# Performance work log

Hardware: AMD Instinct MI355X
Metric: run time of the kernel (lower is better)

Reference implementation:

```python
import jax, jax.numpy as jnp
import numpy as np

D = 1024
H = 16
HD = D // H
T = 2048
B = 2
HID = 4 * D
EPS = 1e-5


def setup_inputs() -> dict:
    key = jax.random.key(0)
    ks = jax.random.split(key, 8)
    s = lambda fan_in: 1.0 / np.sqrt(fan_in)
    return {
        "x": jax.random.normal(ks[0], (B, T, D), dtype=jnp.float32),
        "ln1_g": jnp.ones((D,), jnp.float32),
        "ln1_b": jnp.zeros((D,), jnp.float32),
        "Wqkv": jax.random.uniform(ks[1], (D, 3 * D), jnp.float32, -s(D), s(D)),
        "bqkv": jnp.zeros((3 * D,), jnp.float32),
        "Wout": jax.random.uniform(ks[2], (D, D), jnp.float32, -s(D), s(D)),
        "bout": jnp.zeros((D,), jnp.float32),
        "ln2_g": jnp.ones((D,), jnp.float32),
        "ln2_b": jnp.zeros((D,), jnp.float32),
        "W1": jax.random.uniform(ks[3], (D, HID), jnp.float32, -s(D), s(D)),
        "b1": jnp.zeros((HID,), jnp.float32),
        "W2": jax.random.uniform(ks[4], (HID, D), jnp.float32, -s(HID), s(HID)),
        "b2": jnp.zeros((D,), jnp.float32),
    }


def _layernorm(h, g, b):
    mu = jnp.mean(h, axis=-1, keepdims=True)
    var = jnp.mean(jnp.square(h - mu), axis=-1, keepdims=True)
    return (h - mu) * jax.lax.rsqrt(var + EPS) * g + b


def reference(x, ln1_g, ln1_b, Wqkv, bqkv, Wout, bout, ln2_g, ln2_b, W1, b1, W2, b2):
    b, t, d = x.shape
    scale = 1.0 / np.sqrt(HD)

    # --- attention (pre-LN) ---
    h = _layernorm(x, ln1_g, ln1_b)
    qkv = h @ Wqkv + bqkv                      # [b, t, 3d]
    q, k, v = jnp.split(qkv, 3, axis=-1)
    q = q.reshape(b, t, H, HD)
    k = k.reshape(b, t, H, HD)
    v = v.reshape(b, t, H, HD)
    scores = jnp.einsum("bqhd,bkhd->bhqk", q, k) * scale  # [b, h, t, t]
    causal = jnp.tril(jnp.ones((t, t), dtype=bool))
    scores = jnp.where(causal, scores, -jnp.inf)
    attn = jax.nn.softmax(scores, axis=-1)
    out = jnp.einsum("bhqk,bkhd->bqhd", attn, v).reshape(b, t, d)
    x = x + (out @ Wout + bout)

    # --- MLP (pre-LN) ---
    h = _layernorm(x, ln2_g, ln2_b)
    h = jax.nn.gelu(h @ W1 + b1, approximate=False)
    x = x + (h @ W2 + b2)
    return x
```

## Files before the change

kernel.cpp:

```cpp
#include <hip/hip_runtime.h>
#include <hip/hip_bf16.h>
#include <math.h>

#define DD 1024
#define TT 2048
#define BB 2
#define HH 16
#define HDIM 64
#define HIDD 4096

typedef __attribute__((ext_vector_type(4))) float f32x4;
typedef __attribute__((ext_vector_type(8))) __bf16 bf16x8;
typedef __attribute__((ext_vector_type(4))) __bf16 bf16x4;

#define MF16 __builtin_amdgcn_mfma_f32_16x16x32_bf16

__device__ __forceinline__ void gload_lds16(const void* g, void* l) {
  __builtin_amdgcn_global_load_lds(
      (const __attribute__((address_space(1))) void*)g,
      (__attribute__((address_space(3))) void*)l, 16, 0, 0);
}

__global__ __launch_bounds__(256) void castAll(const float* __restrict__ Wqkv,
                                               const float* __restrict__ Wout,
                                               const float* __restrict__ W1,
                                               const float* __restrict__ W2,
                                               __bf16* __restrict__ WqkvT,
                                               __bf16* __restrict__ WoutT,
                                               __bf16* __restrict__ W1T,
                                               __bf16* __restrict__ W2T) {
  const int id = blockIdx.x;
  const float* W;
  __bf16* Wt;
  int K, N, gx, local;
  if (id < 768)        { W = Wqkv; Wt = WqkvT; K = 1024; N = 3072; gx = 48; local = id; }
  else if (id < 1024)  { W = Wout; Wt = WoutT; K = 1024; N = 1024; gx = 16; local = id - 768; }
  else if (id < 2048)  { W = W1;   Wt = W1T;   K = 1024; N = 4096; gx = 64; local = id - 1024; }
  else                 { W = W2;   Wt = W2T;   K = 4096; N = 1024; gx = 16; local = id - 2048; }
  const int n0 = (local % gx) * 64, k0 = (local / gx) * 64;
  __shared__ float t[64][65];
#pragma unroll
  for (int e = 0; e < 16; ++e) {
    int idx = e * 256 + threadIdx.x;
    int rr = idx >> 6, cc = idx & 63;
    t[rr][cc] = W[(size_t)(k0 + rr) * N + n0 + cc];
  }
  __syncthreads();
#pragma unroll
  for (int e = 0; e < 16; ++e) {
    int idx = e * 256 + threadIdx.x;
    int rr = idx >> 6, cc = idx & 63;
    Wt[(size_t)(n0 + rr) * K + k0 + cc] = (__bf16)t[cc][rr];
  }
}

__global__ __launch_bounds__(256) void ln_fwd(const float* __restrict__ x,
                                              const float* __restrict__ gamma,
                                              const float* __restrict__ beta,
                                              __bf16* __restrict__ out) {
  const int wave = threadIdx.x >> 6, lane = threadIdx.x & 63;
  const int row = blockIdx.x * 4 + wave;
  const float* xr = x + (size_t)row * DD;
  float4 v[4];
  float s = 0.0f, ss = 0.0f;
#pragma unroll
  for (int c = 0; c < 4; ++c) {
    v[c] = reinterpret_cast<const float4*>(xr)[c * 64 + lane];
    s += v[c].x + v[c].y + v[c].z + v[c].w;
    ss += v[c].x * v[c].x + v[c].y * v[c].y + v[c].z * v[c].z + v[c].w * v[c].w;
  }
#pragma unroll
  for (int m = 1; m <= 32; m <<= 1) { s += __shfl_xor(s, m); ss += __shfl_xor(ss, m); }
  const float mu = s * (1.0f / DD);
  const float rs = rsqrtf(ss * (1.0f / DD) - mu * mu + 1e-5f);
#pragma unroll
  for (int c = 0; c < 4; ++c) {
    const float4 gm = reinterpret_cast<const float4*>(gamma)[c * 64 + lane];
    const float4 bt = reinterpret_cast<const float4*>(beta)[c * 64 + lane];
    bf16x4 o;
    o[0] = (__bf16)((v[c].x - mu) * rs * gm.x + bt.x);
    o[1] = (__bf16)((v[c].y - mu) * rs * gm.y + bt.y);
    o[2] = (__bf16)((v[c].z - mu) * rs * gm.z + bt.z);
    o[3] = (__bf16)((v[c].w - mu) * rs * gm.w + bt.w);
    *reinterpret_cast<bf16x4*>(out + (size_t)row * DD + (c * 64 + lane) * 4) = o;
  }
}

template <int MODE, int MAP = 0>
__global__ __launch_bounds__(512, 1) void gemm8(const __bf16* __restrict__ A,
                                                const __bf16* __restrict__ Bt,
                                                const float* __restrict__ bias,
                                                void* __restrict__ out0,
                                                __bf16* __restrict__ q1,
                                                __bf16* __restrict__ q2,
                                                __bf16* __restrict__ q3,
                                                int N, int K, int kchunk) {
  const int tid = threadIdx.x;
  const int wid = tid >> 6, lane = tid & 63;
  const int g = lane >> 4, r = lane & 15;
  const int wrh = wid >> 2;
  const int wc = (wid & 3) * 64;

  int bm, bn, kbase, zz;
  if constexpr (MODE == 3) {
    const int L = blockIdx.x;
    const int xcd = L & 7, idx = L >> 3;
    zz = xcd >> 1;
    bm = (((xcd & 1) << 3) + (idx >> 2)) * 256;
    bn = (idx & 3) * 256;
    kbase = zz * kchunk;
  } else if constexpr (MAP == 1) {
    const int L = blockIdx.x;
    const int xcd = L & 7, idx = L >> 3;
    bm = (((xcd & 1) << 3) + (idx >> 2)) * 256;
    bn = (((xcd >> 1) << 2) + (idx & 3)) * 256;
    kbase = 0;
    zz = 0;
  } else {
    const int gx = gridDim.x;
    const int nwg = gx * gridDim.y;
    const int orig = blockIdx.y * gx + blockIdx.x;
    const int swz = (orig & 7) * (nwg >> 3) + (orig >> 3);
    const int bn4 = swz & 3;
    const int bmt = (swz >> 2) % gx;
    const int bng = (swz >> 2) / gx;
    bm = bmt * 256;
    bn = (bng * 4 + bn4) * 256;
    kbase = 0;
    zz = 0;
  }

  const int NT = kchunk >> 6;
  const __bf16* Asrc = A + (size_t)bm * K + kbase;
  const __bf16* Bsrc = Bt + (size_t)bn * K + kbase;

  __shared__ __bf16 lds[2][4][8192];

  f32x4 acc[8][4] = {};
  bf16x8 bfr[4][2];

  auto STG = [&](int ab, int h, int kt) {
    const __bf16* src = (ab ? Bsrc : Asrc) + (size_t)h * 128 * K;
    char* dst = (char*)&lds[kt & 1][ab * 2 + h][0];
#pragma unroll
    for (int gl = 0; gl < 2; ++gl) {
      const int o = gl * 8192 + wid * 1024 + lane * 16;
      const int row = o >> 7;
      const int cbs = (o & 127) ^ (((row >> 2) & 1) << 5);
      gload_lds16((const char*)src + (size_t)row * (K * 2) + kt * 128 + cbs,
                  dst + gl * 8192 + wid * 1024);
    }
  };
  auto DSA = [&](int s, int mi, int kk) -> bf16x8 {
    return *(const bf16x8*)((const char*)&lds[s][wrh][0] + (mi * 16 + r) * 128 +
                            ((kk * 64 + g * 16) ^ ((r & 4) << 3)));
  };
  auto DSB = [&](int s, int nj, int kk) -> bf16x8 {
    const int rt = wc + nj * 16 + r;
    return *(const bf16x8*)((const char*)&lds[s][2 + (rt >> 7)][0] + (rt & 127) * 128 +
                            ((kk * 64 + g * 16) ^ ((r & 4) << 3)));
  };

#define PH(S, Q, STAGE_STMT, WAIT_STMT)                                        \
  {                                                                            \
    if (Q == 0) {                                                              \
      _Pragma("unroll") for (int nj = 0; nj < 4; ++nj) {                       \
        bfr[nj][0] = DSB(S, nj, 0);                                            \
        bfr[nj][1] = DSB(S, nj, 1);                                            \
      }                                                                        \
    }                                                                          \
    bf16x8 a00 = DSA(S, 2 * Q, 0), a01 = DSA(S, 2 * Q, 1);                     \
    bf16x8 a10 = DSA(S, 2 * Q + 1, 0), a11 = DSA(S, 2 * Q + 1, 1);             \
    STAGE_STMT;                                                                \
    WAIT_STMT;                                                                 \
    __builtin_amdgcn_s_barrier();                                              \
    asm volatile("s_waitcnt lgkmcnt(0)" ::: "memory");                         \
    __builtin_amdgcn_s_setprio(1);                                             \
    _Pragma("unroll") for (int nj = 0; nj < 4; ++nj) {                         \
      acc[2 * Q][nj] = MF16(a00, bfr[nj][0], acc[2 * Q][nj], 0, 0, 0);         \
      acc[2 * Q][nj] = MF16(a01, bfr[nj][1], acc[2 * Q][nj], 0, 0, 0);         \
      acc[2 * Q + 1][nj] = MF16(a10, bfr[nj][0], acc[2 * Q + 1][nj], 0, 0, 0); \
      acc[2 * Q + 1][nj] = MF16(a11, bfr[nj][1], acc[2 * Q + 1][nj], 0, 0, 0); \
    }                                                                          \
    __builtin_amdgcn_s_setprio(0);                                             \
    __builtin_amdgcn_s_barrier();                                              \
  }

  STG(1, 0, 0); STG(1, 1, 0); STG(0, 0, 0); STG(0, 1, 0);
  STG(1, 0, 1); STG(1, 1, 1); STG(0, 0, 1);
  asm volatile("s_waitcnt vmcnt(6)" ::: "memory");
  __builtin_amdgcn_s_barrier();

  const int NI = NT >> 1;
  for (int i = 0; i < NI; ++i) {
    const int k2 = 2 * i + 2, k3 = 2 * i + 3;
    const bool nl = (i + 1 < NI);
    PH(0, 0, { STG(0, 1, 2 * i + 1); }, {});
    PH(0, 1, { if (nl) STG(1, 0, k2); }, {});
    PH(0, 2, { if (nl) STG(1, 1, k2); }, {});
    PH(0, 3, { if (nl) STG(0, 0, k2); },
       { if (nl) asm volatile("s_waitcnt vmcnt(6)" ::: "memory");
         else    asm volatile("s_waitcnt vmcnt(0)" ::: "memory"); });
    PH(1, 0, { if (nl) STG(0, 1, k2); }, {});
    PH(1, 1, { if (nl) STG(1, 0, k3); }, {});
    PH(1, 2, { if (nl) STG(1, 1, k3); }, {});
    PH(1, 3, { if (nl) STG(0, 0, k3); },
       { if (nl) asm volatile("s_waitcnt vmcnt(6)" ::: "memory"); });
  }
#undef PH

  const int row0 = bm + wrh * 128 + g * 4;
  const int col0 = bn + wc + r;
#pragma unroll
  for (int mi = 0; mi < 8; ++mi) {
#pragma unroll
    for (int nj = 0; nj < 4; ++nj) {
      const int col = col0 + nj * 16;
      float bv = 0.0f;
      if constexpr (MODE != 3) bv = bias[col];
#pragma unroll
      for (int i4 = 0; i4 < 4; ++i4) {
        const int rowg = row0 + mi * 16 + i4;
        const size_t idx = (size_t)rowg * N + col;
        const float v = acc[mi][nj][i4];
        if constexpr (MODE == 0) {
          ((__bf16*)out0)[idx] = (__bf16)(v + bv);
        } else if constexpr (MODE == 2) {
          const float t = v + bv;
          const float u2 = t * (1.5957691216f + t * t * 0.0713548163f);
          ((__bf16*)out0)[idx] = (__bf16)(t * __builtin_amdgcn_rcpf(1.0f + __expf(-u2)));
        } else {
          if (zz == 0) {
            ((float*)out0)[idx] = v;
          } else {
            __bf16* p = (zz == 1 ? q1 : (zz == 2 ? q2 : q3));
            p[idx] = (__bf16)v;
          }
        }
      }
    }
  }
}

__global__ __launch_bounds__(256) void reduceW2(const __bf16* __restrict__ p1,
                                                const __bf16* __restrict__ p2,
                                                const __bf16* __restrict__ p3,
                                                const float* __restrict__ x1,
                                                const float* __restrict__ b2,
                                                float* __restrict__ out) {
  const size_t i8 = ((size_t)blockIdx.x * 256 + threadIdx.x) * 8;
  const int col0 = (int)(i8 & 1023);
  bf16x8 a = *(const bf16x8*)(p1 + i8);
  bf16x8 b = *(const bf16x8*)(p2 + i8);
  bf16x8 c = *(const bf16x8*)(p3 + i8);
  float4 o0 = *(const float4*)(out + i8);
  float4 o1 = *(const float4*)(out + i8 + 4);
  const float4 xv0 = *(const float4*)(x1 + i8);
  const float4 xv1 = *(const float4*)(x1 + i8 + 4);
  const float4 bb0 = *(const float4*)(b2 + col0);
  const float4 bb1 = *(const float4*)(b2 + col0 + 4);
  float* op0 = (float*)&o0;
  float* op1 = (float*)&o1;
  const float* xp0 = (const float*)&xv0;
  const float* xp1 = (const float*)&xv1;
  const float* bp0 = (const float*)&bb0;
  const float* bp1 = (const float*)&bb1;
#pragma unroll
  for (int j = 0; j < 4; ++j)
    op0[j] += xp0[j] + bp0[j] + (float)a[j] + (float)b[j] + (float)c[j];
#pragma unroll
  for (int j = 0; j < 4; ++j)
    op1[j] += xp1[j] + bp1[j] + (float)a[4 + j] + (float)b[4 + j] + (float)c[4 + j];
  *(float4*)(out + i8) = o0;
  *(float4*)(out + i8 + 4) = o1;
}

template <int MODE>
__global__ __launch_bounds__(256) void gemm_bt(const __bf16* __restrict__ A,
                                               const __bf16* __restrict__ Bt,
                                               const float* __restrict__ bias,
                                               const float* __restrict__ resid,
                                               void* __restrict__ Cout,
                                               int M, int N, int K) {
  __shared__ __bf16 As[128 * 32];
  __shared__ __bf16 Bs[128 * 32];
  const int tid = threadIdx.x;
  const int wave = tid >> 6, lane = tid & 63;
  const int g = lane >> 4, r = lane & 15;
  const int gx = gridDim.x;
  const int nwg = gx * gridDim.y;
  const int orig = blockIdx.y * gx + blockIdx.x;
  const int swz = (orig & 7) * (nwg >> 3) + (orig >> 3);
  const int bn4 = swz & 3;
  const int bmt = (swz >> 2) % gx;
  const int bng = (swz >> 2) / gx;
  const int bm = bmt * 128;
  const int bn = (bng * 4 + bn4) * 128;
  const int wr = (wave >> 1) * 64, wc = (wave & 1) * 64;
  f32x4 acc[4][4] = {};

  const int off0 = wave * 2048 + lane * 16;
  const int off1 = off0 + 1024;
  const int sr0 = off0 >> 6, sk0 = (off0 & 63) >> 1;
  const int sr1 = off1 >> 6, sk1 = (off1 & 63) >> 1;
  const __bf16* gA0 = A + (size_t)(bm + sr0) * K + sk0;
  const __bf16* gA1 = A + (size_t)(bm + sr1) * K + sk1;
  const __bf16* gB0 = Bt + (size_t)(bn + sr0) * K + sk0;
  const __bf16* gB1 = Bt + (size_t)(bn + sr1) * K + sk1;
  char* lA0 = (char*)As + wave * 2048;
  char* lA1 = lA0 + 1024;
  char* lB0 = (char*)Bs + wave * 2048;
  char* lB1 = lB0 + 1024;

  for (int k0 = 0; k0 < K; k0 += 32) {
    gload_lds16(gA0 + k0, lA0);
    gload_lds16(gA1 + k0, lA1);
    gload_lds16(gB0 + k0, lB0);
    gload_lds16(gB1 + k0, lB1);
    __syncthreads();
    bf16x8 af[4], bf[4];
#pragma unroll
    for (int mi = 0; mi < 4; ++mi)
      af[mi] = *reinterpret_cast<const bf16x8*>(&As[(wr + mi * 16 + r) * 32 + g * 8]);
#pragma unroll
    for (int ni = 0; ni < 4; ++ni)
      bf[ni] = *reinterpret_cast<const bf16x8*>(&Bs[(wc + ni * 16 + r) * 32 + g * 8]);
    __builtin_amdgcn_s_setprio(1);
#pragma unroll
    for (int mi = 0; mi < 4; ++mi)
#pragma unroll
      for (int ni = 0; ni < 4; ++ni)
        acc[mi][ni] = MF16(af[mi], bf[ni], acc[mi][ni], 0, 0, 0);
    __builtin_amdgcn_s_setprio(0);
    __syncthreads();
  }

  const int row0 = bm + wr + 4 * g;
  const int col0 = bn + wc + r;
#pragma unroll
  for (int mi = 0; mi < 4; ++mi) {
#pragma unroll
    for (int ni = 0; ni < 4; ++ni) {
      const int col = col0 + ni * 16;
      const float bv = bias[col];
#pragma unroll
      for (int i = 0; i < 4; ++i) {
        const int row = row0 + mi * 16 + i;
        const size_t idx = (size_t)row * N + col;
        float v = acc[mi][ni][i] + bv;
        if (MODE == 0) {
          ((__bf16*)Cout)[idx] = (__bf16)v;
        } else if (MODE == 1) {
          ((float*)Cout)[idx] = v + resid[idx];
        } else {
          const float u2 = v * (1.5957691216f + v * v * 0.0713548163f);
          const float gl = v * __builtin_amdgcn_rcpf(1.0f + __expf(-u2));
          ((__bf16*)Cout)[idx] = (__bf16)gl;
        }
      }
    }
  }
}

__global__ __launch_bounds__(256) void vtrans(const __bf16* __restrict__ qkv,
                                              __bf16* __restrict__ vtg) {
  const int bh = blockIdx.y, b = bh >> 4, h = bh & 15;
  const int t0 = blockIdx.x * 64;
  const int tid = threadIdx.x, wave = tid >> 6, lane = tid & 63;
  __shared__ __bf16 tile[64 * 64];
#pragma unroll
  for (int e = 0; e < 2; ++e) {
    const int gid = e * 256 + tid;
    const int row = gid >> 3, d0 = (gid & 7) * 8;
    bf16x8 v = *reinterpret_cast<const bf16x8*>(
        qkv + (size_t)(b * TT + t0 + row) * 3072 + 2048 + h * 64 + d0);
    const int slot = (d0 >> 3) ^ (row & 7);
    *reinterpret_cast<bf16x8*>((char*)tile + row * 128 + slot * 16) = v;
  }
  __syncthreads();
  const int d = lane;
#pragma unroll
  for (int e = 0; e < 2; ++e) {
    const int k0 = (wave * 2 + e) * 8;
    bf16x8 o;
#pragma unroll
    for (int j = 0; j < 8; ++j) {
      const int row = k0 + j;
      o[j] = *(const __bf16*)((const char*)tile + row * 128 +
                              (((d >> 3) ^ (row & 7)) << 4) + (d & 7) * 2);
    }
    *reinterpret_cast<bf16x8*>(&vtg[((size_t)bh * 64 + d) * 2048 + t0 + k0]) = o;
  }
}

__device__ __forceinline__ void stage_kv(const __bf16* __restrict__ src_row0, int rstride,
                                         int wave, int lane, char* tile) {
#pragma unroll
  for (int qq = 0; qq < 2; ++qq) {
    const int o = wave * 2048 + qq * 1024 + lane * 16;
    const int p = o >> 12, row = (o >> 6) & 63, cb = (o >> 4) & 3;
    gload_lds16(src_row0 + (size_t)row * rstride + p * 32 + cb * 8,
                tile + wave * 2048 + qq * 1024);
  }
}

__global__ __launch_bounds__(256) void attn_fwd(const __bf16* __restrict__ qkv,
                                                const __bf16* __restrict__ vtg,
                                                __bf16* __restrict__ atto) {
  const int orig = blockIdx.y * gridDim.x + blockIdx.x;
  const int swz = (orig & 7) * 64 + (orig >> 3);
  const int bh = swz >> 4;
  const int j = swz & 15;
  const int b = bh >> 4, h = bh & 15;
  const int tid = threadIdx.x;
  const int wave = tid >> 6, lane = tid & 63;
  const int g = lane >> 4, r = lane & 15;

  __shared__ __bf16 Qs[2 * 64 * 32];
  __shared__ __bf16 Ks[2][2 * 64 * 32];
  __shared__ __bf16 Vs[2][2 * 64 * 32];
  __shared__ __bf16 Pl[4][2 * 16 * 32];

  const __bf16* ksrc = qkv + (size_t)(b * TT) * 3072 + 1024 + h * 64;
  const __bf16* vsrc = vtg + (size_t)bh * 64 * 2048;
  const float C2 = 0.18033688011112042f;

  for (int ph = 0; ph < 2; ++ph) {
    const int qt = ph ? (31 - j) : j;
    const int q0 = qt * 64;
    stage_kv(qkv + (size_t)(b * TT + q0) * 3072 + h * 64, 3072, wave, lane, (char*)Qs);
    stage_kv(ksrc, 3072, wave, lane, (char*)Ks[0]);
    stage_kv(vsrc, 2048, wave, lane, (char*)Vs[0]);

    f32x4 oacc[4] = {};
    float m_s[4], l_s[4];
#pragma unroll
    for (int i = 0; i < 4; ++i) { m_s[i] = -1e30f; l_s[i] = 0.0f; }

    const int nt = qt + 1;
    int cur = 0;
    for (int t = 0; t < nt; ++t) {
      const int kv0 = t * 64;
      __syncthreads();
      if (t + 1 < nt) {
        stage_kv(ksrc + (size_t)(kv0 + 64) * 3072, 3072, wave, lane, (char*)Ks[cur ^ 1]);
        stage_kv(vsrc + kv0 + 64, 2048, wave, lane, (char*)Vs[cur ^ 1]);
      }
      bf16x8 qf[2];
#pragma unroll
      for (int kp = 0; kp < 2; ++kp)
        qf[kp] = *reinterpret_cast<const bf16x8*>(&Qs[kp * 2048 + (wave * 16 + r) * 32 + g * 8]);
      f32x4 s[4];
#pragma unroll
      for (int cn = 0; cn < 4; ++cn) s[cn] = f32x4{0.f, 0.f, 0.f, 0.f};
      __builtin_amdgcn_s_setprio(1);
#pragma unroll
      for (int cn = 0; cn < 4; ++cn)
#pragma unroll
        for (int kp = 0; kp < 2; ++kp) {
          bf16x8 bk = *reinterpret_cast<const bf16x8*>(
              &Ks[cur][kp * 2048 + (cn * 16 + r) * 32 + g * 8]);
          s[cn] = MF16(qf[kp], bk, s[cn], 0, 0, 0);
        }
      __builtin_amdgcn_s_setprio(0);
      const int rowg = q0 + wave * 16 + 4 * g;
      float pm[4];
#pragma unroll
      for (int i = 0; i < 4; ++i) pm[i] = -1e30f;
      if (kv0 + 63 > q0 + wave * 16) {
#pragma unroll
        for (int cn = 0; cn < 4; ++cn) {
          const int colg = kv0 + cn * 16 + r;
#pragma unroll
          for (int i = 0; i < 4; ++i) {
            float v = s[cn][i] * C2;
            v = (colg > rowg + i) ? -1e30f : v;
            s[cn][i] = v;
            pm[i] = fmaxf(pm[i], v);
          }
        }
      } else {
#pragma unroll
        for (int cn = 0; cn < 4; ++cn)
#pragma unroll
          for (int i = 0; i < 4; ++i) {
            const float v = s[cn][i] * C2;
            s[cn][i] = v;
            pm[i] = fmaxf(pm[i], v);
          }
      }
      const int upd = __any((pm[0] > m_s[0] + 8.0f) || (pm[1] > m_s[1] + 8.0f) ||
                            (pm[2] > m_s[2] + 8.0f) || (pm[3] > m_s[3] + 8.0f));
      if (upd) {
#pragma unroll
        for (int i = 0; i < 4; ++i) {
          pm[i] = fmaxf(pm[i], __shfl_xor(pm[i], 1));
          pm[i] = fmaxf(pm[i], __shfl_xor(pm[i], 2));
          pm[i] = fmaxf(pm[i], __shfl_xor(pm[i], 4));
          pm[i] = fmaxf(pm[i], __shfl_xor(pm[i], 8));
          const float mn = fmaxf(m_s[i], pm[i]);
          const float sf = __builtin_amdgcn_exp2f(m_s[i] - mn);
          m_s[i] = mn;
          l_s[i] *= sf;
#pragma unroll
          for (int ni = 0; ni < 4; ++ni) oacc[ni][i] *= sf;
        }
      }
#pragma unroll
      for (int cn = 0; cn < 4; ++cn)
#pragma unroll
        for (int i = 0; i < 4; ++i) {
          const float p = __builtin_amdgcn_exp2f(s[cn][i] - m_s[i]);
          s[cn][i] = p;
          l_s[i] += p;
        }
#pragma unroll
      for (int cn = 0; cn < 4; ++cn)
#pragma unroll
        for (int i = 0; i < 4; ++i) {
          const int row = 4 * g + i;
          const int byteoff = (cn >> 1) * 1024 +
              ((row * 64 + (cn & 1) * 32 + r * 2) ^ ((row & 7) << 4));
          *(__bf16*)((char*)&Pl[wave][0] + byteoff) = (__bf16)s[cn][i];
        }
      bf16x8 pa[2];
#pragma unroll
      for (int kp = 0; kp < 2; ++kp) {
        const int byteoff = kp * 1024 + ((r * 64 + g * 16) ^ ((r & 7) << 4));
        pa[kp] = *reinterpret_cast<const bf16x8*>((const char*)&Pl[wave][0] + byteoff);
      }
      __builtin_amdgcn_s_setprio(1);
#pragma unroll
      for (int ni = 0; ni < 4; ++ni)
#pragma unroll
        for (int kp = 0; kp < 2; ++kp) {
          bf16x8 bv = *reinterpret_cast<const bf16x8*>(
              &Vs[cur][kp * 2048 + (ni * 16 + r) * 32 + g * 8]);
          oacc[ni] = MF16(pa[kp], bv, oacc[ni], 0, 0, 0);
        }
      __builtin_amdgcn_s_setprio(0);
      cur ^= 1;
    }

#pragma unroll
    for (int i = 0; i < 4; ++i) {
      float l = l_s[i];
      l += __shfl_xor(l, 1);
      l += __shfl_xor(l, 2);
      l += __shfl_xor(l, 4);
      l += __shfl_xor(l, 8);
      const float inv = 1.0f / l;
      const size_t rowo = (size_t)(b * TT + q0 + wave * 16 + 4 * g + i) * DD + h * 64;
#pragma unroll
      for (int ni = 0; ni < 4; ++ni)
        atto[rowo + ni * 16 + r] = (__bf16)(oacc[ni][i] * inv);
    }
    __syncthreads();
  }
}

extern "C" void kernel_launch(void* const* d_in, const int* in_sizes, int n_in,
                              void* d_out, int out_size, void* d_ws, size_t ws_size,
                              hipStream_t stream) {
  const float* x     = (const float*)d_in[0];
  const float* ln1_g = (const float*)d_in[1];
  const float* ln1_b = (const float*)d_in[2];
  const float* Wqkv  = (const float*)d_in[3];
  const float* bqkv  = (const float*)d_in[4];
  const float* Wout  = (const float*)d_in[5];
  const float* bout  = (const float*)d_in[6];
  const float* ln2_g = (const float*)d_in[7];
  const float* ln2_b = (const float*)d_in[8];
  const float* W1    = (const float*)d_in[9];
  const float* b1    = (const float*)d_in[10];
  const float* W2    = (const float*)d_in[11];
  const float* b2    = (const float*)d_in[12];
  float* out = (float*)d_out;

  char* ws = (char*)d_ws;
  const size_t MB = 1024 * 1024;
  __bf16* WqkvT = (__bf16*)(ws);
  __bf16* WoutT = (__bf16*)(ws + 6 * MB);
  __bf16* W1T   = (__bf16*)(ws + 8 * MB);
  __bf16* W2T   = (__bf16*)(ws + 16 * MB);
  float*  x1    = (float*)(ws + 24 * MB);
  __bf16* vtg   = (__bf16*)(ws + 24 * MB);
  __bf16* hbuf  = (__bf16*)(ws + 40 * MB);
  __bf16* qkvb  = (__bf16*)(ws + 48 * MB);
  __bf16* atto  = (__bf16*)(ws + 72 * MB);
  __bf16* mlp1  = (__bf16*)(ws + 48 * MB);
  __bf16* p1b   = (__bf16*)(ws);
  __bf16* p2b   = (__bf16*)(ws + 8 * MB);
  __bf16* p3b   = (__bf16*)(ws + 40 * MB);

  castAll<<<3072, 256, 0, stream>>>(Wqkv, Wout, W1, W2, WqkvT, WoutT, W1T, W2T);

  ln_fwd<<<1024, 256, 0, stream>>>(x, ln1_g, ln1_b, hbuf);
  gemm8<0><<<dim3(16, 12), 512, 0, stream>>>(hbuf, WqkvT, bqkv, qkvb,
                                             nullptr, nullptr, nullptr, 3072, 1024, 1024);
  vtrans<<<dim3(32, 32), 256, 0, stream>>>(qkvb, vtg);
  attn_fwd<<<dim3(16, 32), 256, 0, stream>>>(qkvb, vtg, atto);
  gemm_bt<1><<<dim3(32, 8), 256, 0, stream>>>(atto, WoutT, bout, x, x1, 4096, 1024, 1024);

  ln_fwd<<<1024, 256, 0, stream>>>(x1, ln2_g, ln2_b, hbuf);
  gemm8<2, 1><<<256, 512, 0, stream>>>(hbuf, W1T, b1, mlp1,
                                       nullptr, nullptr, nullptr, 4096, 1024, 1024);
  gemm8<3><<<dim3(256, 1), 512, 0, stream>>>(mlp1, W2T, nullptr, out,
                                             p1b, p2b, p3b, 1024, 4096, 1024);
  reduceW2<<<2048, 256, 0, stream>>>(p1b, p2b, p3b, x1, b2, out);
}
```

Before: 232.8 us.

## Replace split-K W2 GEMM with dedicated single-buffered 128x256 tile kernel

Moves the split-K down-projection GEMM off the heavily pipelined 256x256 gemm8 path and into a new gemm_w2 kernel. The new kernel uses 256-thread blocks with 128x256 tiles and a K-step of 32, and launches 512 blocks instead of 256 to get more blocks per CU and better occupancy. It loses the double-buffered LDS pipeline and the swizzled layout, synchronises twice per K step, and its unswizzled LDS reads may cause bank conflicts. gemm8 is simplified by dropping the split-K mode.

Result: slower. 280.3 us (+20.4%).

```diff
diff --git a/kernel.cpp b/kernel.cpp
--- a/kernel.cpp
+++ b/kernel.cpp
@@ -91,9 +91,6 @@
                                                 const __bf16* __restrict__ Bt,
                                                 const float* __restrict__ bias,
                                                 void* __restrict__ out0,
-                                                __bf16* __restrict__ q1,
-                                                __bf16* __restrict__ q2,
-                                                __bf16* __restrict__ q3,
                                                 int N, int K, int kchunk) {
   const int tid = threadIdx.x;
   const int wid = tid >> 6, lane = tid & 63;
@@ -101,21 +98,12 @@
   const int wrh = wid >> 2;
   const int wc = (wid & 3) * 64;
 
-  int bm, bn, kbase, zz;
-  if constexpr (MODE == 3) {
-    const int L = blockIdx.x;
-    const int xcd = L & 7, idx = L >> 3;
-    zz = xcd >> 1;
-    bm = (((xcd & 1) << 3) + (idx >> 2)) * 256;
-    bn = (idx & 3) * 256;
-    kbase = zz * kchunk;
-  } else if constexpr (MAP == 1) {
+  int bm, bn;
+  if constexpr (MAP == 1) {
     const int L = blockIdx.x;
     const int xcd = L & 7, idx = L >> 3;
     bm = (((xcd & 1) << 3) + (idx >> 2)) * 256;
     bn = (((xcd >> 1) << 2) + (idx & 3)) * 256;
-    kbase = 0;
-    zz = 0;
   } else {
     const int gx = gridDim.x;
     const int nwg = gx * gridDim.y;
@@ -126,13 +114,11 @@
     const int bng = (swz >> 2) / gx;
     bm = bmt * 256;
     bn = (bng * 4 + bn4) * 256;
-    kbase = 0;
-    zz = 0;
   }
 
   const int NT = kchunk >> 6;
-  const __bf16* Asrc = A + (size_t)bm * K + kbase;
-  const __bf16* Bsrc = Bt + (size_t)bn * K + kbase;
+  const __bf16* Asrc = A + (size_t)bm * K;
+  const __bf16* Bsrc = Bt + (size_t)bn * K;
 
   __shared__ __bf16 lds[2][4][8192];
 
@@ -216,8 +202,7 @@
 #pragma unroll
     for (int nj = 0; nj < 4; ++nj) {
       const int col = col0 + nj * 16;
-      float bv = 0.0f;
-      if constexpr (MODE != 3) bv = bias[col];
+      const float bv = bias[col];
 #pragma unroll
       for (int i4 = 0; i4 < 4; ++i4) {
         const int rowg = row0 + mi * 16 + i4;
@@ -225,17 +210,99 @@
         const float v = acc[mi][nj][i4];
         if constexpr (MODE == 0) {
           ((__bf16*)out0)[idx] = (__bf16)(v + bv);
-        } else if constexpr (MODE == 2) {
+        } else {
           const float t = v + bv;
           const float u2 = t * (1.5957691216f + t * t * 0.0713548163f);
           ((__bf16*)out0)[idx] = (__bf16)(t * __builtin_amdgcn_rcpf(1.0f + __expf(-u2)));
+        }
+      }
+    }
+  }
+}
+
+__global__ __launch_bounds__(256) void gemm_w2(const __bf16* __restrict__ A,
+                                               const __bf16* __restrict__ Bt,
+                                               void* __restrict__ out0,
+                                               __bf16* __restrict__ q1,
+                                               __bf16* __restrict__ q2,
+                                               __bf16* __restrict__ q3) {
+  const int K = 4096, N = 1024;
+  __shared__ __bf16 As[128 * 32];
+  __shared__ __bf16 Bs[256 * 32];
+  const int tid = threadIdx.x;
+  const int wave = tid >> 6, lane = tid & 63;
+  const int g = lane >> 4, r = lane & 15;
+
+  const int L = blockIdx.x;
+  const int xcd = L & 7, idx = L >> 3;
+  const int zz = xcd >> 1;
+  const int bm = (((xcd & 1) << 4) + (idx >> 2)) * 128;
+  const int bn = (idx & 3) * 256;
+  const int kbase = zz * 1024;
+
+  f32x4 acc[4][8] = {};
+
+  const int off0 = wave * 2048 + lane * 16;
+  const int off1 = off0 + 1024;
+  const int sr0 = off0 >> 6, sk0 = (off0 & 63) >> 1;
+  const int sr1 = off1 >> 6, sk1 = (off1 & 63) >> 1;
+  const __bf16* gA0 = A + (size_t)(bm + sr0) * K + kbase + sk0;
+  const __bf16* gA1 = A + (size_t)(bm + sr1) * K + kbase + sk1;
+  char* lA0 = (char*)As + wave * 2048;
+  char* lA1 = lA0 + 1024;
+  const __bf16* gB[4];
+  char* lB[4];
+#pragma unroll
+  for (int q = 0; q < 4; ++q) {
+    const int ob = wave * 4096 + q * 1024 + lane * 16;
+    const int rb = ob >> 6, kb = (ob & 63) >> 1;
+    gB[q] = Bt + (size_t)(bn + rb) * K + kbase + kb;
+    lB[q] = (char*)Bs + wave * 4096 + q * 1024;
+  }
+
+  const int mh = wave >> 1;
+  const int nh = wave & 1;
+
+  for (int k0 = 0; k0 < 1024; k0 += 32) {
+    gload_lds16(gA0 + k0, lA0);
+    gload_lds16(gA1 + k0, lA1);
+#pragma unroll
+    for (int q = 0; q < 4; ++q) gload_lds16(gB[q] + k0, lB[q]);
+    __syncthreads();
+    bf16x8 af[4], bf[8];
+#pragma unroll
+    for (int mi = 0; mi < 4; ++mi)
+      af[mi] = *reinterpret_cast<const bf16x8*>(&As[(mh * 64 + mi * 16 + r) * 32 + g * 8]);
+#pragma unroll
+    for (int ni = 0; ni < 8; ++ni)
+      bf[ni] = *reinterpret_cast<const bf16x8*>(&Bs[(nh * 128 + ni * 16 + r) * 32 + g * 8]);
+    __builtin_amdgcn_s_setprio(1);
+#pragma unroll
+    for (int mi = 0; mi < 4; ++mi)
+#pragma unroll
+      for (int ni = 0; ni < 8; ++ni)
+        acc[mi][ni] = MF16(af[mi], bf[ni], acc[mi][ni], 0, 0, 0);
+    __builtin_amdgcn_s_setprio(0);
+    __syncthreads();
+  }
+
+  const int row0 = bm + mh * 64 + 4 * g;
+  const int col0 = bn + nh * 128 + r;
+#pragma unroll
+  for (int mi = 0; mi < 4; ++mi) {
+#pragma unroll
+    for (int ni = 0; ni < 8; ++ni) {
+      const int col = col0 + ni * 16;
+#pragma unroll
+      for (int i = 0; i < 4; ++i) {
+        const int row = row0 + mi * 16 + i;
+        const size_t idx2 = (size_t)row * N + col;
+        const float v = acc[mi][ni][i];
+        if (zz == 0) {
+          ((float*)out0)[idx2] = v;
         } else {
-          if (zz == 0) {
-            ((float*)out0)[idx] = v;
-          } else {
-            __bf16* p = (zz == 1 ? q1 : (zz == 2 ? q2 : q3));
-            p[idx] = (__bf16)v;
-          }
+          __bf16* p = (zz == 1 ? q1 : (zz == 2 ? q2 : q3));
+          p[idx2] = (__bf16)v;
         }
       }
     }
@@ -596,16 +663,13 @@
   castAll<<<3072, 256, 0, stream>>>(Wqkv, Wout, W1, W2, WqkvT, WoutT, W1T, W2T);
 
   ln_fwd<<<1024, 256, 0, stream>>>(x, ln1_g, ln1_b, hbuf);
-  gemm8<0><<<dim3(16, 12), 512, 0, stream>>>(hbuf, WqkvT, bqkv, qkvb,
-                                             nullptr, nullptr, nullptr, 3072, 1024, 1024);
+  gemm8<0><<<dim3(16, 12), 512, 0, stream>>>(hbuf, WqkvT, bqkv, qkvb, 3072, 1024, 1024);
   vtrans<<<dim3(32, 32), 256, 0, stream>>>(qkvb, vtg);
   attn_fwd<<<dim3(16, 32), 256, 0, stream>>>(qkvb, vtg, atto);
   gemm_bt<1><<<dim3(32, 8), 256, 0, stream>>>(atto, WoutT, bout, x, x1, 4096, 1024, 1024);
 
   ln_fwd<<<1024, 256, 0, stream>>>(x1, ln2_g, ln2_b, hbuf);
-  gemm8<2, 1><<<256, 512, 0, stream>>>(hbuf, W1T, b1, mlp1,
-                                       nullptr, nullptr, nullptr, 4096, 1024, 1024);
-  gemm8<3><<<dim3(256, 1), 512, 0, stream>>>(mlp1, W2T, nullptr, out,
-                                             p1b, p2b, p3b, 1024, 4096, 1024);
+  gemm8<2, 1><<<256, 512, 0, stream>>>(hbuf, W1T, b1, mlp1, 4096, 1024, 1024);
+  gemm_w2<<<512, 256, 0, stream>>>(mlp1, W2T, out, p1b, p2b, p3b);
   reduceW2<<<2048, 256, 0, stream>>>(p1b, p2b, p3b, x1, b2, out);
 }
```
